# Performance work log

Hardware: AMD Instinct MI355X
Metric: run time of the kernel (lower is better)

Reference implementation:

```python
import jax, jax.numpy as jnp
import numpy as np

# Polynomial coefficients from the original module (hard-coded in forward).
P00, P10, P20, P30 = 0.0, 0.0, 0.0, 0.0      # identity-kernel branch (all zero)
P01, P11, P21 = -0.000287, 0.266, -0.1097    # learned-weight branch
STRIDE, PAD = 1, 1


def _conv(x, w):
    # NCHW input, OIHW kernel -> NCHW output. Equivalent to
    # unfold(x).T @ w.view(O,-1).T reshaped back, i.e. torch's im2col matmul.
    return jax.lax.conv_general_dilated(
        x, w,
        window_strides=(STRIDE, STRIDE),
        padding=[(PAD, PAD), (PAD, PAD)],
        dimension_numbers=('NCHW', 'OIHW', 'NCHW'))


def setup_inputs() -> dict:
    key = jax.random.key(0)
    k1, k2 = jax.random.split(key)
    img = jax.random.normal(k1, (16, 64, 128, 128), dtype=jnp.float32)
    # weights initialized N(0, 0.8) in the original module
    weights = jax.random.normal(k2, (64, 64, 3, 3), dtype=jnp.float32) * 0.8
    identity_kernel = jnp.ones((64, 64, 3, 3), dtype=jnp.float32)
    return {"img": img, "weights": weights, "identity_kernel": identity_kernel}


def reference(img, weights, identity_kernel):
    kh, kw = weights.shape[2], weights.shape[3]
    # Elementwise polynomial applied to the input, then contracted against
    # the (identity, learned) kernels. matmul-with-unfold == convolution,
    # so we express it as two convs instead of materializing im2col.
    poly_id = P00 + P10 * img + P20 * img**2 + P30 * img**3  # == zeros here
    poly_w = P01 + P11 * img + P21 * img**2
    out = _conv(poly_id, identity_kernel) + _conv(poly_w, weights)
    return out / (3 * kh * kw)
```

## Files before the change

kernel.cpp:

```cpp
#include <hip/hip_runtime.h>


typedef __bf16 bf16;
typedef __attribute__((ext_vector_type(8))) __bf16 bf16x8;
typedef __attribute__((ext_vector_type(16))) float f32x16;

static constexpr float A0 = -0.000287f / 27.0f;
static constexpr float A1 =  0.266f    / 27.0f;
static constexpr float A2 = -0.1097f   / 27.0f;

#define NN 16
#define CI 64
#define HH 128
#define WW 128
#define OO 64

__global__ void repack_w(const float* __restrict__ w, bf16* __restrict__ wrb) {
    int idx = blockIdx.x * 256 + threadIdx.x;
    if (idx >= 36864) return;
    int cj    = idx & 7;
    int o     = (idx >> 3) & 63;
    int cc8   = (idx >> 9) & 7;
    int slice = idx >> 12;
    int ky = slice / 3, kx = slice - ky * 3;
    int c = cc8 * 8 + cj;
    wrb[idx] = (bf16)w[((o * CI + c) * 3 + ky) * 3 + kx];
}

__global__ __launch_bounds__(256, 4) void conv_mfma(const float* __restrict__ img,
                                                    const bf16* __restrict__ wrb,
                                                    float* __restrict__ out) {
    __shared__ __align__(16) bf16 ilds[2][8320];

    const int tid  = threadIdx.x;
    const int braw = blockIdx.x;
    const int b    = (braw & 7) * 128 + (braw >> 3);
    const int y0   = (b & 63) * 2;
    const int n    = b >> 6;

    const int wv   = tid >> 6;
    const int lane = tid & 63;
    const int lm   = lane & 31;
    const int half = lane >> 5;
    const int yl   = wv >> 1;
    const int Xh   = (wv & 1) * 64;

    auto stage_load = [&](int chunk, int it, float2* v) {
        const int id = tid + (it << 8);
        const int r = id >> 7, ccl = (id >> 6) & 1, xh = id & 63;
        const int yi = y0 - 1 + r;
        if ((unsigned)yi < 128u) {
            const float* p = img + ((n * CI + chunk * 16 + ccl * 8) * HH + yi) * WW + 2 * xh;
            #pragma unroll
            for (int j = 0; j < 8; ++j) v[j] = *(const float2*)(p + j * HH * WW);
        }
    };
    auto stage_write = [&](int buf, int it, float2* v) {
        const int id = tid + (it << 8);
        const int r = id >> 7, ccl = (id >> 6) & 1, xh = id & 63;
        const int yi = y0 - 1 + r;
        bf16* rowp = &ilds[buf][(r * 2 + ccl) * (130 * 8)];
        bf16x8 pk0, pk1;
        if ((unsigned)yi < 128u) {
            #pragma unroll
            for (int j = 0; j < 8; ++j) {
                pk0[j] = (bf16)(A0 + v[j].x * (A1 + A2 * v[j].x));
                pk1[j] = (bf16)(A0 + v[j].y * (A1 + A2 * v[j].y));
            }
        } else {
            #pragma unroll
            for (int j = 0; j < 8; ++j) { pk0[j] = (bf16)0.0f; pk1[j] = (bf16)0.0f; }
        }
        *(bf16x8*)(rowp + (2 * xh + 1) * 8) = pk0;
        *(bf16x8*)(rowp + (2 * xh + 2) * 8) = pk1;
        if (it == 0 && tid < 8) {
            bf16* hp = &ilds[buf][((tid >> 1) * 2 + (tid & 1)) * (130 * 8)];
            bf16x8 z;
            #pragma unroll
            for (int j = 0; j < 8; ++j) z[j] = (bf16)0.0f;
            *(bf16x8*)(hp + 0) = z;
            *(bf16x8*)(hp + 129 * 8) = z;
        }
    };

    f32x16 acc[2][2];
    #pragma unroll
    for (int i = 0; i < 2; ++i)
        #pragma unroll
        for (int j = 0; j < 2; ++j)
            #pragma unroll
            for (int k = 0; k < 16; ++k) acc[i][j][k] = 0.0f;

    const bf16x8* wfr = (const bf16x8*)wrb;

    {
        float2 v[8];
        stage_load(0, 0, v); stage_write(0, 0, v);
        stage_load(0, 1, v); stage_write(0, 1, v);
    }

    for (int chunk = 0; chunk < 4; ++chunk) {
        __syncthreads();
        float2 v[8];
        if (chunk < 3) stage_load(chunk + 1, 0, v);
        const bf16x8* ifr = (const bf16x8*)ilds[chunk & 1];
        const int cc8g = chunk * 2 + half;
        #pragma unroll
        for (int ky = 0; ky < 3; ++ky) {
            const int r = yl + ky;
            #pragma unroll
            for (int kx = 0; kx < 3; ++kx) {
                const int slice = ky * 3 + kx;
                bf16x8 a0 = wfr[(slice * 8 + cc8g) * 64 + lm];
                bf16x8 a1 = wfr[(slice * 8 + cc8g) * 64 + 32 + lm];
                const int ib = (r * 2 + half) * 130 + Xh + lm + kx;
                bf16x8 b0 = ifr[ib];
                bf16x8 b1 = ifr[ib + 32];
                acc[0][0] = __builtin_amdgcn_mfma_f32_32x32x16_bf16(a0, b0, acc[0][0], 0, 0, 0);
                acc[0][1] = __builtin_amdgcn_mfma_f32_32x32x16_bf16(a0, b1, acc[0][1], 0, 0, 0);
                acc[1][0] = __builtin_amdgcn_mfma_f32_32x32x16_bf16(a1, b0, acc[1][0], 0, 0, 0);
                acc[1][1] = __builtin_amdgcn_mfma_f32_32x32x16_bf16(a1, b1, acc[1][1], 0, 0, 0);
            }
        }
        if (chunk < 3) {
            const int nb = (chunk + 1) & 1;
            stage_write(nb, 0, v);
            stage_load(chunk + 1, 1, v);
            stage_write(nb, 1, v);
        }
    }

    const int ybase = (n * OO * HH + (y0 + yl)) * WW;
    #pragma unroll
    for (int p = 0; p < 2; ++p)
        #pragma unroll
        for (int xt = 0; xt < 2; ++xt) {
            const int x = Xh + xt * 32 + lm;
            #pragma unroll
            for (int rg = 0; rg < 16; ++rg) {
                const int o = (rg & 3) + 8 * (rg >> 2) + 4 * half + 32 * p;
                out[ybase + o * (HH * WW) + x] = acc[p][xt][rg];
            }
        }
}

extern "C" void kernel_launch(void* const* d_in, const int* in_sizes, int n_in,
                              void* d_out, int out_size, void* d_ws, size_t ws_size,
                              hipStream_t stream) {
    const float* img = (const float*)d_in[0];
    const float* w   = (const float*)d_in[1];
    float* out = (float*)d_out;
    bf16* wrb  = (bf16*)d_ws;

    repack_w<<<(36864 + 255) / 256, 256, 0, stream>>>(w, wrb);
    conv_mfma<<<NN * (HH / 2), 256, 0, stream>>>(img, wrb, out);
}
```

Baseline: 130.6 us.

## Stage weights into LDS via direct DMA and double the block to 512 threads

```diff
diff --git a/kernel.cpp b/kernel.cpp
--- a/kernel.cpp
+++ b/kernel.cpp
@@ -17,20 +17,24 @@
 
 __global__ void repack_w(const float* __restrict__ w, bf16* __restrict__ wrb) {
     int idx = blockIdx.x * 256 + threadIdx.x;
-    if (idx >= 36864) return;
-    int cj    = idx & 7;
-    int o     = (idx >> 3) & 63;
-    int cc8   = (idx >> 9) & 7;
-    int slice = idx >> 12;
+    if (idx >= 49152) return;
+    int chunk = idx / 12288;
+    int e     = idx - chunk * 12288;
+    if (e >= 9216) { wrb[idx] = (bf16)0.0f; return; }
+    int cj = e & 7;
+    int o  = (e >> 3) & 63;
+    int sc = e >> 9;
+    int slice = sc >> 1, ccl = sc & 1;
+    int c  = chunk * 16 + ccl * 8 + cj;
     int ky = slice / 3, kx = slice - ky * 3;
-    int c = cc8 * 8 + cj;
     wrb[idx] = (bf16)w[((o * CI + c) * 3 + ky) * 3 + kx];
 }
 
-__global__ __launch_bounds__(256, 4) void conv_mfma(const float* __restrict__ img,
+__global__ __launch_bounds__(512, 4) void conv_mfma(const float* __restrict__ img,
                                                     const bf16* __restrict__ wrb,
                                                     float* __restrict__ out) {
-    __shared__ __align__(16) bf16 ilds[2][8320];
+    __shared__ __align__(16) bf16 stag[2][8320];
+    __shared__ __align__(16) bf16 wlds[12288];
 
     const int tid  = threadIdx.x;
     const int braw = blockIdx.x;
@@ -42,91 +46,122 @@
     const int lane = tid & 63;
     const int lm   = lane & 31;
     const int half = lane >> 5;
-    const int yl   = wv >> 1;
-    const int Xh   = (wv & 1) * 64;
+    const int yl   = wv >> 2;
+    const int Xh   = (wv & 3) * 32;
 
-    auto stage_load = [&](int chunk, int it, float2* v) {
-        const int id = tid + (it << 8);
-        const int r = id >> 7, ccl = (id >> 6) & 1, xh = id & 63;
-        const int yi = y0 - 1 + r;
-        if ((unsigned)yi < 128u) {
-            const float* p = img + ((n * CI + chunk * 16 + ccl * 8) * HH + yi) * WW + 2 * xh;
+    auto sload = [&](int chunk, float2* v) {
+        #pragma unroll
+        for (int rd = 0; rd < 2; ++rd) {
+            const int id  = tid + (rd << 9);
+            const int r   = id / 130;
+            const int rem = id - r * 130;
+            const int ccl = rem / 65;
+            const int xh  = rem - ccl * 65;
+            const int yi  = y0 - 1 + r;
+            const bool ok = (id < 520) && (xh < 64) && ((unsigned)yi < 128u);
+            const float* p = ok ? img + ((n * CI + chunk * 16 + ccl * 8) * HH + yi) * WW + 2 * xh
+                                : img;
             #pragma unroll
-            for (int j = 0; j < 8; ++j) v[j] = *(const float2*)(p + j * HH * WW);
+            for (int j = 0; j < 8; ++j)
+                v[rd * 8 + j] = *(const float2*)(p + (ok ? j * HH * WW : 0));
         }
     };
-    auto stage_write = [&](int buf, int it, float2* v) {
-        const int id = tid + (it << 8);
-        const int r = id >> 7, ccl = (id >> 6) & 1, xh = id & 63;
-        const int yi = y0 - 1 + r;
-        bf16* rowp = &ilds[buf][(r * 2 + ccl) * (130 * 8)];
-        bf16x8 pk0, pk1;
-        if ((unsigned)yi < 128u) {
-            #pragma unroll
-            for (int j = 0; j < 8; ++j) {
-                pk0[j] = (bf16)(A0 + v[j].x * (A1 + A2 * v[j].x));
-                pk1[j] = (bf16)(A0 + v[j].y * (A1 + A2 * v[j].y));
+    auto spack = [&](int buf, float2* v) {
+        #pragma unroll
+        for (int rd = 0; rd < 2; ++rd) {
+            const int id = tid + (rd << 9);
+            if (id >= 520) continue;
+            const int r   = id / 130;
+            const int rem = id - r * 130;
+            const int ccl = rem / 65;
+            const int xh  = rem - ccl * 65;
+            const int yi  = y0 - 1 + r;
+            bf16* rowp = &stag[buf][(r * 2 + ccl) * (130 * 8)];
+            if (xh < 64) {
+                bf16x8 pk0, pk1;
+                if ((unsigned)yi < 128u) {
+                    #pragma unroll
+                    for (int j = 0; j < 8; ++j) {
+                        const float a = v[rd * 8 + j].x, c = v[rd * 8 + j].y;
+                        pk0[j] = (bf16)(A0 + a * (A1 + A2 * a));
+                        pk1[j] = (bf16)(A0 + c * (A1 + A2 * c));
+                    }
+                } else {
+                    #pragma unroll
+                    for (int j = 0; j < 8; ++j) { pk0[j] = (bf16)0.0f; pk1[j] = (bf16)0.0f; }
+                }
+                *(bf16x8*)(rowp + (2 * xh + 1) * 8) = pk0;
+                *(bf16x8*)(rowp + (2 * xh + 2) * 8) = pk1;
+            } else {
+                bf16x8 z;
+                #pragma unroll
+                for (int j = 0; j < 8; ++j) z[j] = (bf16)0.0f;
+                *(bf16x8*)(rowp + 0) = z;
+                *(bf16x8*)(rowp + 129 * 8) = z;
             }
-        } else {
-            #pragma unroll
-            for (int j = 0; j < 8; ++j) { pk0[j] = (bf16)0.0f; pk1[j] = (bf16)0.0f; }
-        }
-        *(bf16x8*)(rowp + (2 * xh + 1) * 8) = pk0;
-        *(bf16x8*)(rowp + (2 * xh + 2) * 8) = pk1;
-        if (it == 0 && tid < 8) {
-            bf16* hp = &ilds[buf][((tid >> 1) * 2 + (tid & 1)) * (130 * 8)];
-            bf16x8 z;
-            #pragma unroll
-            for (int j = 0; j < 8; ++j) z[j] = (bf16)0.0f;
-            *(bf16x8*)(hp + 0) = z;
-            *(bf16x8*)(hp + 129 * 8) = z;
         }
     };
 
-    f32x16 acc[2][2];
+    auto wdma = [&](int c) {
+        #pragma unroll
+        for (int k2 = 0; k2 < 3; ++k2) {
+            const int u = wv + (k2 << 3);
+            const bf16* g = wrb + c * 12288 + u * 512 + lane * 8;
+            __builtin_amdgcn_global_load_lds(
+                (const __attribute__((address_space(1))) void*)g,
+                (__attribute__((address_space(3))) void*)(wlds + u * 512),
+                16, 0, 0);
+        }
+    };
+
+    f32x16 acc[2];
     #pragma unroll
-    for (int i = 0; i < 2; ++i)
-        #pragma unroll
-        for (int j = 0; j < 2; ++j)
-            #pragma unroll
-            for (int k = 0; k < 16; ++k) acc[i][j][k] = 0.0f;
+    for (int k = 0; k < 16; ++k) { acc[0][k] = 0.0f; acc[1][k] = 0.0f; }
 
-    const bf16x8* wfr = (const bf16x8*)wrb;
+    float2 v[16];
 
-    {
-        float2 v[8];
-        stage_load(0, 0, v); stage_write(0, 0, v);
-        stage_load(0, 1, v); stage_write(0, 1, v);
-    }
+    sload(0, v);
+    spack(0, v);
+    wdma(0);
+    sload(1, v);
+    asm volatile("s_waitcnt lgkmcnt(0)" ::: "memory");
+    asm volatile("s_waitcnt vmcnt(16)" ::: "memory");
+    __builtin_amdgcn_sched_barrier(0);
+    __builtin_amdgcn_s_barrier();
+    __builtin_amdgcn_sched_barrier(0);
 
-    for (int chunk = 0; chunk < 4; ++chunk) {
-        __syncthreads();
-        float2 v[8];
-        if (chunk < 3) stage_load(chunk + 1, 0, v);
-        const bf16x8* ifr = (const bf16x8*)ilds[chunk & 1];
-        const int cc8g = chunk * 2 + half;
+    const bf16x8* wptr = (const bf16x8*)wlds;
+
+    for (int k = 0; k < 4; ++k) {
+        const bf16x8* ifr = (const bf16x8*)stag[k & 1];
+        __builtin_amdgcn_s_setprio(1);
         #pragma unroll
         for (int ky = 0; ky < 3; ++ky) {
             const int r = yl + ky;
             #pragma unroll
             for (int kx = 0; kx < 3; ++kx) {
                 const int slice = ky * 3 + kx;
-                bf16x8 a0 = wfr[(slice * 8 + cc8g) * 64 + lm];
-                bf16x8 a1 = wfr[(slice * 8 + cc8g) * 64 + 32 + lm];
-                const int ib = (r * 2 + half) * 130 + Xh + lm + kx;
-                bf16x8 b0 = ifr[ib];
-                bf16x8 b1 = ifr[ib + 32];
-                acc[0][0] = __builtin_amdgcn_mfma_f32_32x32x16_bf16(a0, b0, acc[0][0], 0, 0, 0);
-                acc[0][1] = __builtin_amdgcn_mfma_f32_32x32x16_bf16(a0, b1, acc[0][1], 0, 0, 0);
-                acc[1][0] = __builtin_amdgcn_mfma_f32_32x32x16_bf16(a1, b0, acc[1][0], 0, 0, 0);
-                acc[1][1] = __builtin_amdgcn_mfma_f32_32x32x16_bf16(a1, b1, acc[1][1], 0, 0, 0);
+                bf16x8 a0 = wptr[(slice * 2 + half) * 64 + lm];
+                bf16x8 a1 = wptr[(slice * 2 + half) * 64 + 32 + lm];
+                bf16x8 b0 = ifr[(r * 2 + half) * 130 + Xh + lm + kx];
+                acc[0] = __builtin_amdgcn_mfma_f32_32x32x16_bf16(a0, b0, acc[0], 0, 0, 0);
+                acc[1] = __builtin_amdgcn_mfma_f32_32x32x16_bf16(a1, b0, acc[1], 0, 0, 0);
             }
         }
-        if (chunk < 3) {
-            const int nb = (chunk + 1) & 1;
-            stage_write(nb, 0, v);
-            stage_load(chunk + 1, 1, v);
-            stage_write(nb, 1, v);
+        __builtin_amdgcn_s_setprio(0);
+        if (k < 3) {
+            __builtin_amdgcn_sched_barrier(0);
+            __builtin_amdgcn_s_barrier();
+            __builtin_amdgcn_sched_barrier(0);
+            wdma(k + 1);
+            spack((k + 1) & 1, v);
+            if (k < 2) sload(k + 2, v);
+            asm volatile("s_waitcnt lgkmcnt(0)" ::: "memory");
+            if (k < 2) asm volatile("s_waitcnt vmcnt(16)" ::: "memory");
+            else       asm volatile("s_waitcnt vmcnt(0)"  ::: "memory");
+            __builtin_amdgcn_sched_barrier(0);
+            __builtin_amdgcn_s_barrier();
+            __builtin_amdgcn_sched_barrier(0);
         }
     }
 
@@ -134,13 +169,9 @@
     #pragma unroll
     for (int p = 0; p < 2; ++p)
         #pragma unroll
-        for (int xt = 0; xt < 2; ++xt) {
-            const int x = Xh + xt * 32 + lm;
-            #pragma unroll
-            for (int rg = 0; rg < 16; ++rg) {
-                const int o = (rg & 3) + 8 * (rg >> 2) + 4 * half + 32 * p;
-                out[ybase + o * (HH * WW) + x] = acc[p][xt][rg];
-            }
+        for (int rg = 0; rg < 16; ++rg) {
+            const int o = (rg & 3) + 8 * (rg >> 2) + 4 * half + 32 * p;
+            out[ybase + o * (HH * WW) + Xh + lm] = acc[p][rg];
         }
 }
 
@@ -152,6 +183,6 @@
     float* out = (float*)d_out;
     bf16* wrb  = (bf16*)d_ws;
 
-    repack_w<<<(36864 + 255) / 256, 256, 0, stream>>>(w, wrb);
-    conv_mfma<<<NN * (HH / 2), 256, 0, stream>>>(img, wrb, out);
+    repack_w<<<192, 256, 0, stream>>>(w, wrb);
+    conv_mfma<<<NN * (HH / 2), 512, 0, stream>>>(img, wrb, out);
 }
```

Result: slower. 196.9 us (+50.8%).
